# Kernel optimization log

Hardware: AMD Instinct MI355X
Metric: run time of the kernel (lower is better)

## Reference

```python
import jax, jax.numpy as jnp
import numpy as np

D_MODEL = 2048
N_HEADS = 16
HEAD_DIM = D_MODEL // N_HEADS  # 128
BASE = 10000.0
NEG = -1e9


def _rope_tables(seq_len, dtype=jnp.float32):
    # inv_freq over even dims of head_dim, emb = cat(freqs, freqs)
    inv_freq = 1.0 / (BASE ** (jnp.arange(0, HEAD_DIM, 2, dtype=jnp.float32) / HEAD_DIM))
    t = jnp.arange(seq_len, dtype=jnp.float32)
    freqs = jnp.einsum('i,j->ij', t, inv_freq)          # [S, hd/2]
    emb = jnp.concatenate([freqs, freqs], axis=-1)       # [S, hd]
    return jnp.cos(emb).astype(dtype)[None, None], jnp.sin(emb).astype(dtype)[None, None]


def _rotate_half(x):
    # Faithful to source: rotary_ndims == head_dim, so x2 is empty and this returns x.
    x1, x2 = x[..., :HEAD_DIM], x[..., HEAD_DIM:]
    return jnp.concatenate([-x2, x1], axis=-1)


def setup_inputs() -> dict:
    key = jax.random.key(0)
    ks = jax.random.split(key, 5)
    B, S = 2, 2048
    x = jax.random.normal(ks[0], (B, S, D_MODEL), dtype=jnp.float32)
    # additive causal mask [1,1,S,S]
    causal = jnp.tril(jnp.ones((S, S), dtype=bool))
    attention_mask = jnp.where(causal, 0.0, NEG).astype(jnp.float32)[None, None]
    scale = 1.0 / np.sqrt(D_MODEL)
    Wq = jax.random.normal(ks[1], (D_MODEL, D_MODEL), dtype=jnp.float32) * scale
    Wk = jax.random.normal(ks[2], (D_MODEL, D_MODEL), dtype=jnp.float32) * scale
    Wv = jax.random.normal(ks[3], (D_MODEL, D_MODEL), dtype=jnp.float32) * scale
    Wd = jax.random.normal(ks[4], (D_MODEL, D_MODEL), dtype=jnp.float32) * scale
    return {"x": x, "attention_mask": attention_mask, "Wq": Wq, "Wk": Wk, "Wv": Wv, "Wd": Wd}


def reference(x, attention_mask, Wq, Wk, Wv, Wd):
    B, S, _ = x.shape
    # torch Linear: y = x @ W.T  (weights stored [out, in])
    def proj(W):
        y = jnp.einsum('bsd,ed->bse', x, W)
        return y.reshape(B, S, N_HEADS, HEAD_DIM).transpose(0, 2, 1, 3)  # [B,H,S,hd]
    q, k, v = proj(Wq), proj(Wk), proj(Wv)
    cos, sin = _rope_tables(S, x.dtype)
    q = q * cos + _rotate_half(q) * sin
    k = k * cos + _rotate_half(k) * sin
    scores = jnp.einsum('bhqd,bhkd->bhqk', q, k) / jnp.sqrt(jnp.float32(HEAD_DIM)).astype(x.dtype)
    scores = scores + attention_mask
    attn = jax.nn.softmax(scores, axis=-1)
    out = jnp.einsum('bhqk,bhkd->bhqd', attn, v)
    out = out.transpose(0, 2, 1, 3).reshape(B, S, D_MODEL)
    return jnp.einsum('bse,de->bsd', out, Wd)
```

## Files before the change

### kernel.cpp

```cpp
#include <hip/hip_runtime.h>
#include <stdint.h>

#define DM   2048
#define NH   16
#define HD   128
#define BB   2
#define SS   2048
#define MM   (BB*SS)
#define KK   2048
#define NQKV (3*DM)

#define LOG2E  1.4426950408889634f
#define SCALE  0.08838834764831845f

using bf16x8 = __attribute__((ext_vector_type(8))) __bf16;
using f32x4  = __attribute__((ext_vector_type(4))) float;
typedef unsigned short u16;
typedef unsigned int   u32;

__device__ __forceinline__ u16 f2bf(float f) {
  u32 u = __float_as_uint(f);
  u32 r = (u + 0x7FFFu + ((u >> 16) & 1u)) >> 16;
  return (u16)r;
}

__device__ __forceinline__ void load_lds16(const void* g, void* l) {
  __builtin_amdgcn_global_load_lds(
      (__attribute__((address_space(1))) void*)(g),
      (__attribute__((address_space(3))) void*)(l), 16, 0, 0);
}

__global__ void cast_f32_bf16(const float* __restrict__ s, u16* __restrict__ d, int n) {
  int i = (blockIdx.x * blockDim.x + threadIdx.x) * 4;
  if (i < n) {
    float4 f = *(const float4*)(s + i);
    u32 lo = (u32)f2bf(f.x) | ((u32)f2bf(f.y) << 16);
    u32 hi = (u32)f2bf(f.z) | ((u32)f2bf(f.w) << 16);
    *(uint2*)(d + i) = make_uint2(lo, hi);
  }
}

__global__ void rope_fct(float* __restrict__ f) {
  int i = blockIdx.x * blockDim.x + threadIdx.x;
  if (i < SS * 128) {
    int s = i >> 7, j = i & 127;
    double inv = pow(10000.0, -(double)(j & 63) / 64.0);
    float ang = (float)s * (float)inv;
    float sn, cs;
    sincosf(ang, &sn, &cs);
    f[i] = cs + sn;
  }
}


__device__ __forceinline__ void stage_unit(const u16* __restrict__ G, int rowbase,
                                           int kbase, u16* lds, int tid) {
#pragma unroll
  for (int i = 0; i < 2; i++) {
    int s = i * 512 + tid;
    int r = s >> 3, c = s & 7;
    load_lds16(G + (size_t)(rowbase + r) * KK + kbase + ((c ^ (r & 7)) * 8),
               (char*)lds + (size_t)s * 16);
  }
}

#define COLN(ni) (((ni) < 2) ? (wn * 32 + (ni) * 16) : (128 + wn * 32 + ((ni) - 2) * 16))

#define GEMM_MAIN_LOOP                                                          \
  const int tid = threadIdx.x;                                                  \
  const int wid = tid >> 6, lane = tid & 63, ln = lane & 15, quad = lane >> 4;  \
  const int wm = wid >> 2, wn = wid & 3;                                        \
  const int m0 = blockIdx.x * 128, n0 = blockIdx.y * 256;                       \
  const f32x4 fz = {0.f, 0.f, 0.f, 0.f};                                        \
  f32x4 acc[4][4];                                                              \
  _Pragma("unroll") for (int mi = 0; mi < 4; mi++)                              \
    _Pragma("unroll") for (int ni = 0; ni < 4; ni++) acc[mi][ni] = fz;          \
  int aRow[4], bRow[4];                                                         \
  _Pragma("unroll") for (int mi = 0; mi < 4; mi++)                              \
    aRow[mi] = wm * 64 + mi * 16 + ln;                                          \
  _Pragma("unroll") for (int ni = 0; ni < 4; ni++)                              \
    bRow[ni] = COLN(ni) + ln;                                                   \
                            \
  stage_unit(A, m0, 0, Sh, tid);                                                \
  stage_unit(Bm, n0, 0, Sh + 16384, tid);                                       \
  stage_unit(Bm, n0 + 128, 0, Sh + 16384 + 8192, tid);                          \
  const int nT = KK / 64;                                                       \
  for (int t = 0; t < nT; t++) {                                                \
    const int cur = t & 1;                                                      \
    const u16* At = Sh + cur * 8192;                                            \
    const u16* Bt = Sh + 16384 + cur * 16384;                                   \
    u16* Ax = Sh + (cur ^ 1) * 8192;                                            \
    u16* Bx = Sh + 16384 + (cur ^ 1) * 16384;                                   \
    const int kn = (t + 1) * 64;                                                \
    const bool nl = (t + 1 < nT);                                               \
    bf16x8 aF[2][4], bF[2][2];                                                  \
                              \
    __asm__ __volatile__("s_waitcnt vmcnt(2)" ::: "memory");                    \
    __asm__ __volatile__("s_barrier" ::: "memory");                             \
    _Pragma("unroll") for (int kk = 0; kk < 2; kk++) {                          \
      _Pragma("unroll") for (int mi = 0; mi < 4; mi++)                          \
        aF[kk][mi] = *(const bf16x8*)&At[aRow[mi] * 64 +                        \
                      (((kk * 4 + quad) ^ (aRow[mi] & 7)) * 8)];                \
      _Pragma("unroll") for (int ni = 0; ni < 2; ni++)                          \
        bF[kk][ni] = *(const bf16x8*)&Bt[bRow[ni] * 64 +                        \
                      (((kk * 4 + quad) ^ (bRow[ni] & 7)) * 8)];                \
    }                                                                           \
    if (nl) {                                                                   \
      stage_unit(A, m0, kn, Ax, tid);                                           \
      stage_unit(Bm, n0, kn, Bx, tid);                                          \
    }                                                                           \
    __asm__ __volatile__("s_waitcnt lgkmcnt(0)" ::: "memory");                  \
    __builtin_amdgcn_sched_barrier(0);                                          \
    __builtin_amdgcn_s_setprio(1);                                              \
    _Pragma("unroll") for (int kk = 0; kk < 2; kk++)                            \
      _Pragma("unroll") for (int mi = 0; mi < 4; mi++)                          \
        _Pragma("unroll") for (int ni = 0; ni < 2; ni++)                        \
          acc[mi][ni] = __builtin_amdgcn_mfma_f32_16x16x32_bf16(                \
              aF[kk][mi], bF[kk][ni], acc[mi][ni], 0, 0, 0);                    \
    __builtin_amdgcn_s_setprio(0);                                              \
    __builtin_amdgcn_sched_barrier(0);                                          \
                         \
    if (nl) { __asm__ __volatile__("s_waitcnt vmcnt(4)" ::: "memory"); }        \
    else    { __asm__ __volatile__("s_waitcnt vmcnt(0)" ::: "memory"); }        \
    __asm__ __volatile__("s_barrier" ::: "memory");                             \
    _Pragma("unroll") for (int kk = 0; kk < 2; kk++)                            \
      _Pragma("unroll") for (int ni = 0; ni < 2; ni++)                          \
        bF[kk][ni] = *(const bf16x8*)&Bt[bRow[2 + ni] * 64 +                    \
                      (((kk * 4 + quad) ^ (bRow[2 + ni] & 7)) * 8)];            \
    if (nl) stage_unit(Bm, n0 + 128, kn, Bx + 8192, tid);                       \
    __asm__ __volatile__("s_waitcnt lgkmcnt(0)" ::: "memory");                  \
    __builtin_amdgcn_sched_barrier(0);                                          \
    __builtin_amdgcn_s_setprio(1);                                              \
    _Pragma("unroll") for (int kk = 0; kk < 2; kk++)                            \
      _Pragma("unroll") for (int mi = 0; mi < 4; mi++)                          \
        _Pragma("unroll") for (int ni = 0; ni < 2; ni++)                        \
          acc[mi][2 + ni] = __builtin_amdgcn_mfma_f32_16x16x32_bf16(            \
              aF[kk][mi], bF[kk][ni], acc[mi][2 + ni], 0, 0, 0);                \
    __builtin_amdgcn_s_setprio(0);                                              \
    __builtin_amdgcn_sched_barrier(0);                                          \
  }

__global__ __launch_bounds__(512, 2)
void gemm_qkv_rope(const u16* __restrict__ A, const u16* __restrict__ Bm,
                   u16* __restrict__ qo, u16* __restrict__ ko, u16* __restrict__ vo,
                   const float* __restrict__ fct) {
  __shared__ __align__(16) u16 Sh[49152];
  GEMM_MAIN_LOOP

  const int tensor = n0 >> 11;
  const int h0 = (n0 & 2047) >> 7;
  if (tensor < 2) {
    u16* dst = (tensor == 0) ? qo : ko;
#pragma unroll
    for (int mi = 0; mi < 4; mi++) {
      int rowM = wm * 64 + mi * 16;
#pragma unroll
      for (int r = 0; r < 4; r++) {
        int m = m0 + rowM + quad * 4 + r;
        int b = m >> 11, s = m & 2047;
        const float* fr = fct + s * 128;
#pragma unroll
        for (int ni = 0; ni < 4; ni++) {
          int colN = COLN(ni) + ln;
          int h = h0 + (colN >> 7);
          int j = colN & 127;
          dst[((size_t)(b * NH + h) * SS + s) * HD + j] = f2bf(acc[mi][ni][r] * fr[j]);
        }
      }
    }
  } else {
    __syncthreads();
    u16* Tr = Sh;
    const int b = m0 >> 11, s0 = m0 & 2047;
#pragma unroll
    for (int mi = 0; mi < 4; mi++) {
      int rowM = wm * 64 + mi * 16;
#pragma unroll
      for (int ni = 0; ni < 4; ni++) {
        int colN = COLN(ni) + ln;
#pragma unroll
        for (int r = 0; r < 4; r++) {
          int srel = rowM + quad * 4 + r;
          int ch = srel >> 3;
          Tr[colN * 128 + ((ch ^ (colN & 15)) * 8) + (srel & 7)] = f2bf(acc[mi][ni][r]);
        }
      }
    }
    __syncthreads();
#pragma unroll
    for (int it = 0; it < 8; it++) {
      int slot = it * 512 + tid;
      int nloc = slot >> 4, c8 = slot & 15;
      uint4 val = *(const uint4*)&Tr[nloc * 128 + ((c8 ^ (nloc & 15)) * 8)];
      int h = h0 + (nloc >> 7), hd = nloc & 127;
      *(uint4*)(vo + ((size_t)(b * NH + h) * HD + hd) * SS + s0 + c8 * 8) = val;
    }
  }
}

__global__ __launch_bounds__(512, 2)
void gemm_out(const u16* __restrict__ A, const u16* __restrict__ Bm,
              float* __restrict__ C) {
  __shared__ __align__(16) u16 Sh[49152];
  GEMM_MAIN_LOOP

#pragma unroll
  for (int mi = 0; mi < 4; mi++) {
    int rowM = wm * 64 + mi * 16;
#pragma unroll
    for (int r = 0; r < 4; r++) {
      int m = m0 + rowM + quad * 4 + r;
#pragma unroll
      for (int ni = 0; ni < 4; ni++) {
        int colN = COLN(ni) + ln;
        C[(size_t)m * DM + n0 + colN] = acc[mi][ni][r];
      }
    }
  }
}

__global__ __launch_bounds__(256, 2)
void flash_attn(const u16* __restrict__ q, const u16* __restrict__ k,
                const u16* __restrict__ v, u16* __restrict__ o) {
  __shared__ __align__(16) u16 Ps[64 * 64];
  __shared__ __align__(16) u16 Ks[2][64 * 128];
  __shared__ __align__(16) u16 Vs[2][128 * 64];
  const int tid = threadIdx.x;
  const int w = tid >> 6, lane = tid & 63, ln = lane & 15, quad = lane >> 4;
  const int hh = blockIdx.y, b = blockIdx.z;
  const size_t bh = (size_t)b * NH + hh;
  const u16* Kg = k + bh * SS * HD;
  const u16* Vg = v + bh * HD * SS;

  for (int half = 0; half < 2; half++) {
    const int T = half ? (31 - (int)blockIdx.x) : (int)blockIdx.x;
    const u16* Qg = q + bh * SS * HD + (size_t)T * 64 * HD;

    bf16x8 qf[4];
#pragma unroll
    for (int kc = 0; kc < 4; kc++)
      qf[kc] = *(const bf16x8*)(Qg + (size_t)(w * 16 + ln) * HD + (kc * 4 + quad) * 8);

    __syncthreads();

#pragma unroll
    for (int i = 0; i < 4; i++) {
      int slot = i * 256 + tid;
      int r = slot >> 4, c = (slot & 15) ^ (r & 7);
      load_lds16(Kg + (size_t)r * HD + c * 8, (char*)Ks[0] + slot * 16);
    }
#pragma unroll
    for (int i = 0; i < 4; i++) {
      int slot = i * 256 + tid;
      int r = slot >> 3, c = (slot & 7) ^ (r & 7);
      load_lds16(Vg + (size_t)r * SS + c * 8, (char*)Vs[0] + slot * 16);
    }

    const f32x4 fz = {0.f, 0.f, 0.f, 0.f};
    float m_s[4], l_s[4];
    f32x4 accO[8];
#pragma unroll
    for (int r = 0; r < 4; r++) { m_s[r] = -1e30f; l_s[r] = 0.f; }
#pragma unroll
    for (int nt = 0; nt < 8; nt++) accO[nt] = fz;

    const int nkt = T + 1;
    const int qrb = T * 64 + w * 16;

    for (int kt = 0; kt < nkt; kt++) {
      const int cur = kt & 1;
      const int k0 = kt * 64;
      __asm__ __volatile__("s_waitcnt vmcnt(0)" ::: "memory");
      __syncthreads();
      if (kt + 1 < nkt) {
        const int kn = k0 + 64;
#pragma unroll
        for (int i = 0; i < 4; i++) {
          int slot = i * 256 + tid;
          int r = slot >> 4, c = (slot & 15) ^ (r & 7);
          load_lds16(Kg + (size_t)(kn + r) * HD + c * 8, (char*)Ks[cur ^ 1] + slot * 16);
        }
#pragma unroll
        for (int i = 0; i < 4; i++) {
          int slot = i * 256 + tid;
          int r = slot >> 3, c = (slot & 7) ^ (r & 7);
          load_lds16(Vg + (size_t)r * SS + kn + c * 8, (char*)Vs[cur ^ 1] + slot * 16);
        }
      }

      f32x4 sc[4];
#pragma unroll
      for (int nt = 0; nt < 4; nt++) sc[nt] = fz;
#pragma unroll
      for (int kc = 0; kc < 4; kc++)
#pragma unroll
        for (int nt = 0; nt < 4; nt++) {
          bf16x8 bf = *(const bf16x8*)&Ks[cur][(nt * 16 + ln) * 128 + (((kc * 4 + quad) ^ (ln & 7)) * 8)];
          sc[nt] = __builtin_amdgcn_mfma_f32_16x16x32_bf16(qf[kc], bf, sc[nt], 0, 0, 0);
        }

      const bool partial = (kt == T);
#pragma unroll
      for (int nt = 0; nt < 4; nt++)
#pragma unroll
        for (int r = 0; r < 4; r++) {
          float val = sc[nt][r] * SCALE;
          if (partial && (k0 + nt * 16 + ln > qrb + quad * 4 + r)) val = -1e9f;
          sc[nt][r] = val;
        }

#pragma unroll
      for (int r = 0; r < 4; r++) {
        float mx = fmaxf(fmaxf(sc[0][r], sc[1][r]), fmaxf(sc[2][r], sc[3][r]));
#pragma unroll
        for (int off = 1; off < 16; off <<= 1) mx = fmaxf(mx, __shfl_xor(mx, off));
        float mnew = fmaxf(m_s[r], mx);
        float alpha = exp2f((m_s[r] - mnew) * LOG2E);
        float rs = 0.f;
#pragma unroll
        for (int nt = 0; nt < 4; nt++) {
          float p = exp2f((sc[nt][r] - mnew) * LOG2E);
          sc[nt][r] = p;
          rs += p;
        }
#pragma unroll
        for (int off = 1; off < 16; off <<= 1) rs += __shfl_xor(rs, off);
        l_s[r] = l_s[r] * alpha + rs;
        m_s[r] = mnew;
#pragma unroll
        for (int nt = 0; nt < 8; nt++) accO[nt][r] *= alpha;
      }

#pragma unroll
      for (int nt = 0; nt < 4; nt++)
#pragma unroll
        for (int r = 0; r < 4; r++) {
          int rr = w * 16 + quad * 4 + r;
          int j = nt * 16 + ln;
          Ps[rr * 64 + (((j >> 3) ^ (rr & 7)) * 8) + (j & 7)] = f2bf(sc[nt][r]);
        }
      __asm__ __volatile__("s_waitcnt lgkmcnt(0)" ::: "memory");

      bf16x8 pf[2];
#pragma unroll
      for (int kc = 0; kc < 2; kc++) {
        int rp = w * 16 + ln;
        pf[kc] = *(const bf16x8*)&Ps[rp * 64 + (((kc * 4 + quad) ^ (ln & 7)) * 8)];
      }

#pragma unroll
      for (int kc = 0; kc < 2; kc++)
#pragma unroll
        for (int nt = 0; nt < 8; nt++) {
          bf16x8 vf = *(const bf16x8*)&Vs[cur][(nt * 16 + ln) * 64 + (((kc * 4 + quad) ^ (ln & 7)) * 8)];
          accO[nt] = __builtin_amdgcn_mfma_f32_16x16x32_bf16(pf[kc], vf, accO[nt], 0, 0, 0);
        }
    }

#pragma unroll
    for (int r = 0; r < 4; r++) {
      float ilv = 1.f / l_s[r];
      int srow = T * 64 + w * 16 + quad * 4 + r;
      size_t base = ((size_t)b * SS + srow) * DM + hh * HD;
#pragma unroll
      for (int nt = 0; nt < 8; nt++)
        o[base + nt * 16 + ln] = f2bf(accO[nt][r] * ilv);
    }
  }
}

extern "C" void kernel_launch(void* const* d_in, const int* in_sizes, int n_in,
                              void* d_out, int out_size, void* d_ws, size_t ws_size,
                              hipStream_t stream) {
  (void)in_sizes; (void)n_in; (void)out_size; (void)ws_size;
  const float* x  = (const float*)d_in[0];
  const float* Wq = (const float*)d_in[2];
  const float* Wk = (const float*)d_in[3];
  const float* Wv = (const float*)d_in[4];
  const float* Wd = (const float*)d_in[5];

  char* ws = (char*)d_ws;
  u16* xb   = (u16*)(ws);
  u16* aob  = xb;
  u16* wqkv = (u16*)(ws + 16777216ull);
  float* fct = (float*)(ws + 41943040ull);
  u16* wdb  = (u16*)(ws + 41943040ull);
  u16* qb   = (u16*)(ws + 50331648ull);
  u16* kb   = (u16*)(ws + 67108864ull);
  u16* vtb  = (u16*)(ws + 83886080ull);

  cast_f32_bf16<<<8192, 256, 0, stream>>>(x,  xb, MM * KK);
  cast_f32_bf16<<<4096, 256, 0, stream>>>(Wq, wqkv,                   DM * KK);
  cast_f32_bf16<<<4096, 256, 0, stream>>>(Wk, wqkv + (size_t)DM*KK,   DM * KK);
  cast_f32_bf16<<<4096, 256, 0, stream>>>(Wv, wqkv + (size_t)2*DM*KK, DM * KK);
  rope_fct<<<1024, 256, 0, stream>>>(fct);

  gemm_qkv_rope<<<dim3(MM / 128, NQKV / 256), 512, 0, stream>>>(xb, wqkv, qb, kb, vtb, fct);

  cast_f32_bf16<<<4096, 256, 0, stream>>>(Wd, wdb, DM * KK);

  flash_attn<<<dim3(16, NH, BB), 256, 0, stream>>>(qb, kb, vtb, aob);
  gemm_out<<<dim3(MM / 128, DM / 256), 512, 0, stream>>>(aob, wdb, (float*)d_out);
}
```

Before: 391.0 us.

## Fold softmax scale into Q, give each attention wave two query tiles, lazily rescale

The QKV GEMM epilogue now multiplies Q by scale*log2e, so the attention kernel can drop the per-score multiply and use exp2 directly. The flash-attention block shrinks to 2 waves, each owning 32 query rows as two 16-row MFMA tiles, so each K/V fragment read from LDS is reused twice. Online softmax skips the max update and accumulator rescale unless some row's max grows by more than 8 (log2 units). The costs are more registers per wave, half as many waves per block to hide latency, and the lazy rescale risking slightly different numerics.

```diff
diff --git a/kernel.cpp b/kernel.cpp
--- a/kernel.cpp
+++ b/kernel.cpp
@@ -12,6 +12,7 @@
 
 #define LOG2E  1.4426950408889634f
 #define SCALE  0.08838834764831845f
+#define QKSC   (SCALE * LOG2E)
 
 using bf16x8 = __attribute__((ext_vector_type(8))) __bf16;
 using f32x4  = __attribute__((ext_vector_type(4))) float;
@@ -151,6 +152,7 @@
   const int h0 = (n0 & 2047) >> 7;
   if (tensor < 2) {
     u16* dst = (tensor == 0) ? qo : ko;
+    const float qsc = (tensor == 0) ? (float)QKSC : 1.0f;
 #pragma unroll
     for (int mi = 0; mi < 4; mi++) {
       int rowM = wm * 64 + mi * 16;
@@ -164,7 +166,7 @@
           int colN = COLN(ni) + ln;
           int h = h0 + (colN >> 7);
           int j = colN & 127;
-          dst[((size_t)(b * NH + h) * SS + s) * HD + j] = f2bf(acc[mi][ni][r] * fr[j]);
+          dst[((size_t)(b * NH + h) * SS + s) * HD + j] = f2bf(acc[mi][ni][r] * fr[j] * qsc);
         }
       }
     }
@@ -219,7 +221,7 @@
   }
 }
 
-__global__ __launch_bounds__(256, 2)
+__global__ __launch_bounds__(128, 2)
 void flash_attn(const u16* __restrict__ q, const u16* __restrict__ k,
                 const u16* __restrict__ v, u16* __restrict__ o) {
   __shared__ __align__(16) u16 Ps[64 * 64];
@@ -236,36 +238,40 @@
     const int T = half ? (31 - (int)blockIdx.x) : (int)blockIdx.x;
     const u16* Qg = q + bh * SS * HD + (size_t)T * 64 * HD;
 
-    bf16x8 qf[4];
-#pragma unroll
-    for (int kc = 0; kc < 4; kc++)
-      qf[kc] = *(const bf16x8*)(Qg + (size_t)(w * 16 + ln) * HD + (kc * 4 + quad) * 8);
+    bf16x8 qf[2][4];
+#pragma unroll
+    for (int mt = 0; mt < 2; mt++)
+#pragma unroll
+      for (int kc = 0; kc < 4; kc++)
+        qf[mt][kc] = *(const bf16x8*)(Qg + (size_t)(w * 32 + mt * 16 + ln) * HD + (kc * 4 + quad) * 8);
 
     __syncthreads();
 
 #pragma unroll
-    for (int i = 0; i < 4; i++) {
-      int slot = i * 256 + tid;
+    for (int i = 0; i < 8; i++) {
+      int slot = i * 128 + tid;
       int r = slot >> 4, c = (slot & 15) ^ (r & 7);
       load_lds16(Kg + (size_t)r * HD + c * 8, (char*)Ks[0] + slot * 16);
     }
 #pragma unroll
-    for (int i = 0; i < 4; i++) {
-      int slot = i * 256 + tid;
+    for (int i = 0; i < 8; i++) {
+      int slot = i * 128 + tid;
       int r = slot >> 3, c = (slot & 7) ^ (r & 7);
       load_lds16(Vg + (size_t)r * SS + c * 8, (char*)Vs[0] + slot * 16);
     }
 
     const f32x4 fz = {0.f, 0.f, 0.f, 0.f};
-    float m_s[4], l_s[4];
-    f32x4 accO[8];
-#pragma unroll
-    for (int r = 0; r < 4; r++) { m_s[r] = -1e30f; l_s[r] = 0.f; }
-#pragma unroll
-    for (int nt = 0; nt < 8; nt++) accO[nt] = fz;
+    float m_s[2][4], l_s[2][4];
+    f32x4 accO[2][8];
+#pragma unroll
+    for (int mt = 0; mt < 2; mt++) {
+#pragma unroll
+      for (int r = 0; r < 4; r++) { m_s[mt][r] = -1e30f; l_s[mt][r] = 0.f; }
+#pragma unroll
+      for (int nt = 0; nt < 8; nt++) accO[mt][nt] = fz;
+    }
 
     const int nkt = T + 1;
-    const int qrb = T * 64 + w * 16;
 
     for (int kt = 0; kt < nkt; kt++) {
       const int cur = kt & 1;
@@ -275,97 +281,143 @@
       if (kt + 1 < nkt) {
         const int kn = k0 + 64;
 #pragma unroll
-        for (int i = 0; i < 4; i++) {
-          int slot = i * 256 + tid;
+        for (int i = 0; i < 8; i++) {
+          int slot = i * 128 + tid;
           int r = slot >> 4, c = (slot & 15) ^ (r & 7);
           load_lds16(Kg + (size_t)(kn + r) * HD + c * 8, (char*)Ks[cur ^ 1] + slot * 16);
         }
 #pragma unroll
-        for (int i = 0; i < 4; i++) {
-          int slot = i * 256 + tid;
+        for (int i = 0; i < 8; i++) {
+          int slot = i * 128 + tid;
           int r = slot >> 3, c = (slot & 7) ^ (r & 7);
           load_lds16(Vg + (size_t)r * SS + kn + c * 8, (char*)Vs[cur ^ 1] + slot * 16);
         }
       }
 
-      f32x4 sc[4];
-#pragma unroll
-      for (int nt = 0; nt < 4; nt++) sc[nt] = fz;
+      f32x4 sc[2][4];
+#pragma unroll
+      for (int mt = 0; mt < 2; mt++)
+#pragma unroll
+        for (int nt = 0; nt < 4; nt++) sc[mt][nt] = fz;
 #pragma unroll
       for (int kc = 0; kc < 4; kc++)
 #pragma unroll
         for (int nt = 0; nt < 4; nt++) {
           bf16x8 bf = *(const bf16x8*)&Ks[cur][(nt * 16 + ln) * 128 + (((kc * 4 + quad) ^ (ln & 7)) * 8)];
-          sc[nt] = __builtin_amdgcn_mfma_f32_16x16x32_bf16(qf[kc], bf, sc[nt], 0, 0, 0);
-        }
-
-      const bool partial = (kt == T);
-#pragma unroll
-      for (int nt = 0; nt < 4; nt++)
+#pragma unroll
+          for (int mt = 0; mt < 2; mt++)
+            sc[mt][nt] = __builtin_amdgcn_mfma_f32_16x16x32_bf16(qf[mt][kc], bf, sc[mt][nt], 0, 0, 0);
+        }
+
+      if (kt == T) {
+#pragma unroll
+        for (int mt = 0; mt < 2; mt++)
+#pragma unroll
+          for (int nt = 0; nt < 4; nt++)
+#pragma unroll
+            for (int r = 0; r < 4; r++)
+              if (k0 + nt * 16 + ln > T * 64 + w * 32 + mt * 16 + quad * 4 + r)
+                sc[mt][nt][r] = -1e9f;
+      }
+
+      float mx[2][4];
+#pragma unroll
+      for (int mt = 0; mt < 2; mt++)
 #pragma unroll
         for (int r = 0; r < 4; r++) {
-          float val = sc[nt][r] * SCALE;
-          if (partial && (k0 + nt * 16 + ln > qrb + quad * 4 + r)) val = -1e9f;
-          sc[nt][r] = val;
-        }
-
-#pragma unroll
-      for (int r = 0; r < 4; r++) {
-        float mx = fmaxf(fmaxf(sc[0][r], sc[1][r]), fmaxf(sc[2][r], sc[3][r]));
-#pragma unroll
-        for (int off = 1; off < 16; off <<= 1) mx = fmaxf(mx, __shfl_xor(mx, off));
-        float mnew = fmaxf(m_s[r], mx);
-        float alpha = exp2f((m_s[r] - mnew) * LOG2E);
-        float rs = 0.f;
-#pragma unroll
-        for (int nt = 0; nt < 4; nt++) {
-          float p = exp2f((sc[nt][r] - mnew) * LOG2E);
-          sc[nt][r] = p;
-          rs += p;
-        }
-#pragma unroll
-        for (int off = 1; off < 16; off <<= 1) rs += __shfl_xor(rs, off);
-        l_s[r] = l_s[r] * alpha + rs;
-        m_s[r] = mnew;
-#pragma unroll
-        for (int nt = 0; nt < 8; nt++) accO[nt][r] *= alpha;
-      }
-
-#pragma unroll
-      for (int nt = 0; nt < 4; nt++)
-#pragma unroll
-        for (int r = 0; r < 4; r++) {
-          int rr = w * 16 + quad * 4 + r;
-          int j = nt * 16 + ln;
-          Ps[rr * 64 + (((j >> 3) ^ (rr & 7)) * 8) + (j & 7)] = f2bf(sc[nt][r]);
-        }
+          float m0x = fmaxf(fmaxf(sc[mt][0][r], sc[mt][1][r]), fmaxf(sc[mt][2][r], sc[mt][3][r]));
+#pragma unroll
+          for (int off = 1; off < 16; off <<= 1) m0x = fmaxf(m0x, __shfl_xor(m0x, off));
+          mx[mt][r] = m0x;
+        }
+      bool need = false;
+#pragma unroll
+      for (int mt = 0; mt < 2; mt++)
+#pragma unroll
+        for (int r = 0; r < 4; r++) need |= (mx[mt][r] > m_s[mt][r] + 8.f);
+
+      if (__any(need)) {
+#pragma unroll
+        for (int mt = 0; mt < 2; mt++)
+#pragma unroll
+          for (int r = 0; r < 4; r++) {
+            float mnew = fmaxf(m_s[mt][r], mx[mt][r]);
+            float alpha = exp2f(m_s[mt][r] - mnew);
+            float rs = 0.f;
+#pragma unroll
+            for (int nt = 0; nt < 4; nt++) {
+              float p = exp2f(sc[mt][nt][r] - mnew);
+              sc[mt][nt][r] = p;
+              rs += p;
+            }
+#pragma unroll
+            for (int off = 1; off < 16; off <<= 1) rs += __shfl_xor(rs, off);
+            l_s[mt][r] = l_s[mt][r] * alpha + rs;
+            m_s[mt][r] = mnew;
+#pragma unroll
+            for (int nt = 0; nt < 8; nt++) accO[mt][nt][r] *= alpha;
+          }
+      } else {
+#pragma unroll
+        for (int mt = 0; mt < 2; mt++)
+#pragma unroll
+          for (int r = 0; r < 4; r++) {
+            float rs = 0.f;
+#pragma unroll
+            for (int nt = 0; nt < 4; nt++) {
+              float p = exp2f(sc[mt][nt][r] - m_s[mt][r]);
+              sc[mt][nt][r] = p;
+              rs += p;
+            }
+#pragma unroll
+            for (int off = 1; off < 16; off <<= 1) rs += __shfl_xor(rs, off);
+            l_s[mt][r] += rs;
+          }
+      }
+
+#pragma unroll
+      for (int mt = 0; mt < 2; mt++)
+#pragma unroll
+        for (int nt = 0; nt < 4; nt++)
+#pragma unroll
+          for (int r = 0; r < 4; r++) {
+            int rr = w * 32 + mt * 16 + quad * 4 + r;
+            int j = nt * 16 + ln;
+            Ps[rr * 64 + (((j >> 3) ^ (rr & 7)) * 8) + (j & 7)] = f2bf(sc[mt][nt][r]);
+          }
       __asm__ __volatile__("s_waitcnt lgkmcnt(0)" ::: "memory");
 
-      bf16x8 pf[2];
-#pragma unroll
-      for (int kc = 0; kc < 2; kc++) {
-        int rp = w * 16 + ln;
-        pf[kc] = *(const bf16x8*)&Ps[rp * 64 + (((kc * 4 + quad) ^ (ln & 7)) * 8)];
-      }
+      bf16x8 pf[2][2];
+#pragma unroll
+      for (int mt = 0; mt < 2; mt++)
+#pragma unroll
+        for (int kc = 0; kc < 2; kc++) {
+          int rp = w * 32 + mt * 16 + ln;
+          pf[mt][kc] = *(const bf16x8*)&Ps[rp * 64 + (((kc * 4 + quad) ^ (ln & 7)) * 8)];
+        }
 
 #pragma unroll
       for (int kc = 0; kc < 2; kc++)
 #pragma unroll
         for (int nt = 0; nt < 8; nt++) {
           bf16x8 vf = *(const bf16x8*)&Vs[cur][(nt * 16 + ln) * 64 + (((kc * 4 + quad) ^ (ln & 7)) * 8)];
-          accO[nt] = __builtin_amdgcn_mfma_f32_16x16x32_bf16(pf[kc], vf, accO[nt], 0, 0, 0);
-        }
-    }
-
-#pragma unroll
-    for (int r = 0; r < 4; r++) {
-      float ilv = 1.f / l_s[r];
-      int srow = T * 64 + w * 16 + quad * 4 + r;
-      size_t base = ((size_t)b * SS + srow) * DM + hh * HD;
-#pragma unroll
-      for (int nt = 0; nt < 8; nt++)
-        o[base + nt * 16 + ln] = f2bf(accO[nt][r] * ilv);
-    }
+#pragma unroll
+          for (int mt = 0; mt < 2; mt++)
+            accO[mt][nt] = __builtin_amdgcn_mfma_f32_16x16x32_bf16(pf[mt][kc], vf, accO[mt][nt], 0, 0, 0);
+        }
+    }
+
+#pragma unroll
+    for (int mt = 0; mt < 2; mt++)
+#pragma unroll
+      for (int r = 0; r < 4; r++) {
+        float ilv = 1.f / l_s[mt][r];
+        int srow = T * 64 + w * 32 + mt * 16 + quad * 4 + r;
+        size_t base = ((size_t)b * SS + srow) * DM + hh * HD;
+#pragma unroll
+        for (int nt = 0; nt < 8; nt++)
+          o[base + nt * 16 + ln] = f2bf(accO[mt][nt][r] * ilv);
+      }
   }
 }
 
@@ -399,6 +451,6 @@
 
   cast_f32_bf16<<<4096, 256, 0, stream>>>(Wd, wdb, DM * KK);
 
-  flash_attn<<<dim3(16, NH, BB), 256, 0, stream>>>(qb, kb, vtb, aob);
+  flash_attn<<<dim3(16, NH, BB), 128, 0, stream>>>(qb, kb, vtb, aob);
   gemm_out<<<dim3(MM / 128, DM / 256), 512, 0, stream>>>(aob, wdb, (float*)d_out);
 }
```

New measurement: 437.3 us. 11.9% more time.

## Fold softmax scale into Q, add lazy max rescaling and MFMA priority hints

Applied to the files above, without the earlier changes.

The softmax scale and log2(e) factor are folded into Q in the QKV projection epilogue, so the attention loop can call exp2 directly on scores without per-element multiplies. The online softmax now rescales the running max and output accumulator only when some row's new max exceeds the stored max by more than 8 (in log2 units), chosen wave-uniformly. Otherwise it skips the alpha exponentials and the 32 accumulator multiplies per row. s_setprio hints are also placed around both MFMA blocks to favour matrix-core issue across waves. The lazy rescale lets unnormalised exponentials grow up to 2^8, and rounding Q to bf16 after scaling slightly changes numerics.

```diff
diff --git a/kernel.cpp b/kernel.cpp
--- a/kernel.cpp
+++ b/kernel.cpp
@@ -12,6 +12,7 @@
 
 #define LOG2E  1.4426950408889634f
 #define SCALE  0.08838834764831845f
+#define QKSC   (SCALE * LOG2E)
 
 using bf16x8 = __attribute__((ext_vector_type(8))) __bf16;
 using f32x4  = __attribute__((ext_vector_type(4))) float;
@@ -151,6 +152,7 @@
   const int h0 = (n0 & 2047) >> 7;
   if (tensor < 2) {
     u16* dst = (tensor == 0) ? qo : ko;
+    const float qsc = (tensor == 0) ? (float)QKSC : 1.0f;
 #pragma unroll
     for (int mi = 0; mi < 4; mi++) {
       int rowM = wm * 64 + mi * 16;
@@ -164,7 +166,7 @@
           int colN = COLN(ni) + ln;
           int h = h0 + (colN >> 7);
           int j = colN & 127;
-          dst[((size_t)(b * NH + h) * SS + s) * HD + j] = f2bf(acc[mi][ni][r] * fr[j]);
+          dst[((size_t)(b * NH + h) * SS + s) * HD + j] = f2bf(acc[mi][ni][r] * fr[j] * qsc);
         }
       }
     }
@@ -291,6 +293,7 @@
       f32x4 sc[4];
 #pragma unroll
       for (int nt = 0; nt < 4; nt++) sc[nt] = fz;
+      __builtin_amdgcn_s_setprio(1);
 #pragma unroll
       for (int kc = 0; kc < 4; kc++)
 #pragma unroll
@@ -298,37 +301,61 @@
           bf16x8 bf = *(const bf16x8*)&Ks[cur][(nt * 16 + ln) * 128 + (((kc * 4 + quad) ^ (ln & 7)) * 8)];
           sc[nt] = __builtin_amdgcn_mfma_f32_16x16x32_bf16(qf[kc], bf, sc[nt], 0, 0, 0);
         }
-
-      const bool partial = (kt == T);
-#pragma unroll
-      for (int nt = 0; nt < 4; nt++)
+      __builtin_amdgcn_s_setprio(0);
+
+      if (kt == T) {
+#pragma unroll
+        for (int nt = 0; nt < 4; nt++)
+#pragma unroll
+          for (int r = 0; r < 4; r++)
+            if (k0 + nt * 16 + ln > qrb + quad * 4 + r) sc[nt][r] = -1e9f;
+      }
+
+      float mx[4];
+#pragma unroll
+      for (int r = 0; r < 4; r++) {
+        float m0x = fmaxf(fmaxf(sc[0][r], sc[1][r]), fmaxf(sc[2][r], sc[3][r]));
+#pragma unroll
+        for (int off = 1; off < 16; off <<= 1) m0x = fmaxf(m0x, __shfl_xor(m0x, off));
+        mx[r] = m0x;
+      }
+      bool need = false;
+#pragma unroll
+      for (int r = 0; r < 4; r++) need |= (mx[r] > m_s[r] + 8.f);
+
+      if (__any(need)) {
 #pragma unroll
         for (int r = 0; r < 4; r++) {
-          float val = sc[nt][r] * SCALE;
-          if (partial && (k0 + nt * 16 + ln > qrb + quad * 4 + r)) val = -1e9f;
-          sc[nt][r] = val;
-        }
-
-#pragma unroll
-      for (int r = 0; r < 4; r++) {
-        float mx = fmaxf(fmaxf(sc[0][r], sc[1][r]), fmaxf(sc[2][r], sc[3][r]));
-#pragma unroll
-        for (int off = 1; off < 16; off <<= 1) mx = fmaxf(mx, __shfl_xor(mx, off));
-        float mnew = fmaxf(m_s[r], mx);
-        float alpha = exp2f((m_s[r] - mnew) * LOG2E);
-        float rs = 0.f;
-#pragma unroll
-        for (int nt = 0; nt < 4; nt++) {
-          float p = exp2f((sc[nt][r] - mnew) * LOG2E);
-          sc[nt][r] = p;
-          rs += p;
-        }
-#pragma unroll
-        for (int off = 1; off < 16; off <<= 1) rs += __shfl_xor(rs, off);
-        l_s[r] = l_s[r] * alpha + rs;
-        m_s[r] = mnew;
-#pragma unroll
-        for (int nt = 0; nt < 8; nt++) accO[nt][r] *= alpha;
+          float mnew = fmaxf(m_s[r], mx[r]);
+          float alpha = exp2f(m_s[r] - mnew);
+          float rs = 0.f;
+#pragma unroll
+          for (int nt = 0; nt < 4; nt++) {
+            float p = exp2f(sc[nt][r] - mnew);
+            sc[nt][r] = p;
+            rs += p;
+          }
+#pragma unroll
+          for (int off = 1; off < 16; off <<= 1) rs += __shfl_xor(rs, off);
+          l_s[r] = l_s[r] * alpha + rs;
+          m_s[r] = mnew;
+#pragma unroll
+          for (int nt = 0; nt < 8; nt++) accO[nt][r] *= alpha;
+        }
+      } else {
+#pragma unroll
+        for (int r = 0; r < 4; r++) {
+          float rs = 0.f;
+#pragma unroll
+          for (int nt = 0; nt < 4; nt++) {
+            float p = exp2f(sc[nt][r] - m_s[r]);
+            sc[nt][r] = p;
+            rs += p;
+          }
+#pragma unroll
+          for (int off = 1; off < 16; off <<= 1) rs += __shfl_xor(rs, off);
+          l_s[r] += rs;
+        }
       }
 
 #pragma unroll
@@ -348,6 +375,7 @@
         pf[kc] = *(const bf16x8*)&Ps[rp * 64 + (((kc * 4 + quad) ^ (ln & 7)) * 8)];
       }
 
+      __builtin_amdgcn_s_setprio(1);
 #pragma unroll
       for (int kc = 0; kc < 2; kc++)
 #pragma unroll
@@ -355,6 +383,7 @@
           bf16x8 vf = *(const bf16x8*)&Vs[cur][(nt * 16 + ln) * 64 + (((kc * 4 + quad) ^ (ln & 7)) * 8)];
           accO[nt] = __builtin_amdgcn_mfma_f32_16x16x32_bf16(pf[kc], vf, accO[nt], 0, 0, 0);
         }
+      __builtin_amdgcn_s_setprio(0);
     }
 
 #pragma unroll
```

After: 394.3 us. About the same (+0.9%).

## Streamline flash attention softmax with lazy rescale, MFMA row sums, and XCD-aware mapping

Applied to the files above, without the earlier changes.

Folds the softmax scale and log2e into Q during the QKV GEMM epilogue, so the attention loop no longer multiplies scores and calls exp2 directly. The running-max rescale of the accumulators is skipped unless some row's max grows by more than a threshold. Row sums are computed with MFMA against a vector of ones instead of shuffle reductions. It also adds s_setprio around the MFMA blocks and remaps blocks to a 1D grid so each (batch, head) group is scheduled on a single XCD. The lazy rescale relies on the bf16/fp32 range holding values up to 2^8 above the stored max.

```diff
diff --git a/kernel.cpp b/kernel.cpp
--- a/kernel.cpp
+++ b/kernel.cpp
@@ -12,6 +12,7 @@
 
 #define LOG2E  1.4426950408889634f
 #define SCALE  0.08838834764831845f
+#define QKSC   (SCALE * LOG2E)
 
 using bf16x8 = __attribute__((ext_vector_type(8))) __bf16;
 using f32x4  = __attribute__((ext_vector_type(4))) float;
@@ -151,6 +152,7 @@
   const int h0 = (n0 & 2047) >> 7;
   if (tensor < 2) {
     u16* dst = (tensor == 0) ? qo : ko;
+    const float qsc = (tensor == 0) ? (float)QKSC : 1.0f;
 #pragma unroll
     for (int mi = 0; mi < 4; mi++) {
       int rowM = wm * 64 + mi * 16;
@@ -164,7 +166,7 @@
           int colN = COLN(ni) + ln;
           int h = h0 + (colN >> 7);
           int j = colN & 127;
-          dst[((size_t)(b * NH + h) * SS + s) * HD + j] = f2bf(acc[mi][ni][r] * fr[j]);
+          dst[((size_t)(b * NH + h) * SS + s) * HD + j] = f2bf(acc[mi][ni][r] * fr[j] * qsc);
         }
       }
     }
@@ -227,13 +229,21 @@
   __shared__ __align__(16) u16 Vs[2][128 * 64];
   const int tid = threadIdx.x;
   const int w = tid >> 6, lane = tid & 63, ln = lane & 15, quad = lane >> 4;
-  const int hh = blockIdx.y, b = blockIdx.z;
+  const int L = blockIdx.x;
+  const int cxcd = L & 7, qq = L >> 3;
+  const int g = ((qq >> 4) << 3) + cxcd;
+  const int bx = qq & 15;
+  const int hh = g & 15, b = g >> 4;
   const size_t bh = (size_t)b * NH + hh;
   const u16* Kg = k + bh * SS * HD;
   const u16* Vg = v + bh * HD * SS;
 
+  bf16x8 ones;
+#pragma unroll
+  for (int i = 0; i < 8; i++) ones[i] = (__bf16)1.0f;
+
   for (int half = 0; half < 2; half++) {
-    const int T = half ? (31 - (int)blockIdx.x) : (int)blockIdx.x;
+    const int T = half ? (31 - bx) : bx;
     const u16* Qg = q + bh * SS * HD + (size_t)T * 64 * HD;
 
     bf16x8 qf[4];
@@ -257,10 +267,11 @@
     }
 
     const f32x4 fz = {0.f, 0.f, 0.f, 0.f};
-    float m_s[4], l_s[4];
+    float m_s[4];
+    f32x4 accL = fz;
     f32x4 accO[8];
 #pragma unroll
-    for (int r = 0; r < 4; r++) { m_s[r] = -1e30f; l_s[r] = 0.f; }
+    for (int r = 0; r < 4; r++) m_s[r] = -1e30f;
 #pragma unroll
     for (int nt = 0; nt < 8; nt++) accO[nt] = fz;
 
@@ -291,6 +302,7 @@
       f32x4 sc[4];
 #pragma unroll
       for (int nt = 0; nt < 4; nt++) sc[nt] = fz;
+      __builtin_amdgcn_s_setprio(1);
 #pragma unroll
       for (int kc = 0; kc < 4; kc++)
 #pragma unroll
@@ -298,46 +310,46 @@
           bf16x8 bf = *(const bf16x8*)&Ks[cur][(nt * 16 + ln) * 128 + (((kc * 4 + quad) ^ (ln & 7)) * 8)];
           sc[nt] = __builtin_amdgcn_mfma_f32_16x16x32_bf16(qf[kc], bf, sc[nt], 0, 0, 0);
         }
-
-      const bool partial = (kt == T);
+      __builtin_amdgcn_s_setprio(0);
+
+      if (kt == T) {
+#pragma unroll
+        for (int nt = 0; nt < 4; nt++)
+#pragma unroll
+          for (int r = 0; r < 4; r++)
+            if (k0 + nt * 16 + ln > qrb + quad * 4 + r) sc[nt][r] = -1e9f;
+      }
+
+      float lmx[4];
+      bool need = false;
+#pragma unroll
+      for (int r = 0; r < 4; r++) {
+        lmx[r] = fmaxf(fmaxf(sc[0][r], sc[1][r]), fmaxf(sc[2][r], sc[3][r]));
+        need |= (lmx[r] > m_s[r] + 8.f);
+      }
+      if (__any(need)) {
+#pragma unroll
+        for (int r = 0; r < 4; r++) {
+          float mx = lmx[r];
+#pragma unroll
+          for (int off = 1; off < 16; off <<= 1) mx = fmaxf(mx, __shfl_xor(mx, off));
+          float mnew = fmaxf(m_s[r], mx);
+          float alpha = exp2f(m_s[r] - mnew);
+          m_s[r] = mnew;
+          accL[r] *= alpha;
+#pragma unroll
+          for (int nt = 0; nt < 8; nt++) accO[nt][r] *= alpha;
+        }
+      }
+
 #pragma unroll
       for (int nt = 0; nt < 4; nt++)
 #pragma unroll
         for (int r = 0; r < 4; r++) {
-          float val = sc[nt][r] * SCALE;
-          if (partial && (k0 + nt * 16 + ln > qrb + quad * 4 + r)) val = -1e9f;
-          sc[nt][r] = val;
-        }
-
-#pragma unroll
-      for (int r = 0; r < 4; r++) {
-        float mx = fmaxf(fmaxf(sc[0][r], sc[1][r]), fmaxf(sc[2][r], sc[3][r]));
-#pragma unroll
-        for (int off = 1; off < 16; off <<= 1) mx = fmaxf(mx, __shfl_xor(mx, off));
-        float mnew = fmaxf(m_s[r], mx);
-        float alpha = exp2f((m_s[r] - mnew) * LOG2E);
-        float rs = 0.f;
-#pragma unroll
-        for (int nt = 0; nt < 4; nt++) {
-          float p = exp2f((sc[nt][r] - mnew) * LOG2E);
-          sc[nt][r] = p;
-          rs += p;
-        }
-#pragma unroll
-        for (int off = 1; off < 16; off <<= 1) rs += __shfl_xor(rs, off);
-        l_s[r] = l_s[r] * alpha + rs;
-        m_s[r] = mnew;
-#pragma unroll
-        for (int nt = 0; nt < 8; nt++) accO[nt][r] *= alpha;
-      }
-
-#pragma unroll
-      for (int nt = 0; nt < 4; nt++)
-#pragma unroll
-        for (int r = 0; r < 4; r++) {
+          __bf16 pb = (__bf16)exp2f(sc[nt][r] - m_s[r]);
           int rr = w * 16 + quad * 4 + r;
           int j = nt * 16 + ln;
-          Ps[rr * 64 + (((j >> 3) ^ (rr & 7)) * 8) + (j & 7)] = f2bf(sc[nt][r]);
+          Ps[rr * 64 + (((j >> 3) ^ (rr & 7)) * 8) + (j & 7)] = *(u16*)&pb;
         }
       __asm__ __volatile__("s_waitcnt lgkmcnt(0)" ::: "memory");
 
@@ -348,6 +360,7 @@
         pf[kc] = *(const bf16x8*)&Ps[rp * 64 + (((kc * 4 + quad) ^ (ln & 7)) * 8)];
       }
 
+      __builtin_amdgcn_s_setprio(1);
 #pragma unroll
       for (int kc = 0; kc < 2; kc++)
 #pragma unroll
@@ -355,11 +368,14 @@
           bf16x8 vf = *(const bf16x8*)&Vs[cur][(nt * 16 + ln) * 64 + (((kc * 4 + quad) ^ (ln & 7)) * 8)];
           accO[nt] = __builtin_amdgcn_mfma_f32_16x16x32_bf16(pf[kc], vf, accO[nt], 0, 0, 0);
         }
+      accL = __builtin_amdgcn_mfma_f32_16x16x32_bf16(pf[0], ones, accL, 0, 0, 0);
+      accL = __builtin_amdgcn_mfma_f32_16x16x32_bf16(pf[1], ones, accL, 0, 0, 0);
+      __builtin_amdgcn_s_setprio(0);
     }
 
 #pragma unroll
     for (int r = 0; r < 4; r++) {
-      float ilv = 1.f / l_s[r];
+      float ilv = 1.f / accL[r];
       int srow = T * 64 + w * 16 + quad * 4 + r;
       size_t base = ((size_t)b * SS + srow) * DM + hh * HD;
 #pragma unroll
@@ -399,6 +415,6 @@
 
   cast_f32_bf16<<<4096, 256, 0, stream>>>(Wd, wdb, DM * KK);
 
-  flash_attn<<<dim3(16, NH, BB), 256, 0, stream>>>(qb, kb, vtb, aob);
+  flash_attn<<<512, 256, 0, stream>>>(qb, kb, vtb, aob);
   gemm_out<<<dim3(MM / 128, DM / 256), 512, 0, stream>>>(aob, wdb, (float*)d_out);
 }
```

New measurement: 366.3 us. -6.3%, faster.
